# Kernel optimization log

Measured on AMD Instinct MI355X. Metric: run time of the kernel, lower is better.

The kernel has to match this reference:

```python
import jax, jax.numpy as jnp
import numpy as np

EPS = 1e-5

def _dynconv1x1(x, f):
    # x: [B, Cin, H, W], f: [B, Cout, Cin, 1, 1] -> [B, Cout, H, W]
    return jnp.einsum('bchw,boc->bohw', x, f[..., 0, 0])

def _instance_norm(x):
    # per-sample, per-channel normalization over spatial dims (no affine)
    mu = jnp.mean(x, axis=(2, 3), keepdims=True)
    var = jnp.mean(jnp.square(x - mu), axis=(2, 3), keepdims=True)
    return (x - mu) / jnp.sqrt(var + EPS)

def setup_inputs() -> dict:
    key = jax.random.key(0)
    ks = jax.random.split(key, 10)
    B, C = 32, 128
    sizes = [128, 64, 32, 16, 8]
    inp = {}
    for i, s in enumerate(sizes):
        inp[f'x{i+1}'] = jax.random.normal(ks[i], (B, C, s, s), dtype=jnp.float32)
        inp[f'l{i+1}fs'] = jax.random.normal(ks[5 + i], (B, C, C, 1, 1), dtype=jnp.float32) * 0.05
    return inp

def reference(x1, x2, x3, x4, x5, l1fs, l2fs, l3fs, l4fs, l5fs):
    y1 = _instance_norm(_dynconv1x1(x1, l1fs))
    y2 = _instance_norm(_dynconv1x1(x2, l2fs))
    y3 = _instance_norm(_dynconv1x1(x3, l3fs))
    y4 = _instance_norm(_dynconv1x1(x4, l4fs))
    y5 = _dynconv1x1(x5, l5fs)  # level 5 has no norm in the original
    return (y1, y2, y3, y4, y5)
```

## Files before the change

kernel.cpp:

```cpp
#include <hip/hip_runtime.h>
#include <stdint.h>


typedef __bf16 bf16x8 __attribute__((ext_vector_type(8)));
typedef float f32x4 __attribute__((ext_vector_type(4)));
typedef unsigned short u16;
typedef u16 u16x4 __attribute__((ext_vector_type(4)));
typedef u16 u16x8 __attribute__((ext_vector_type(8)));

__device__ __forceinline__ u16 f2bf(float f) {
    uint32_t u = __builtin_bit_cast(uint32_t, f);
    u += 0x7fffu + ((u >> 16) & 1u);
    return (u16)(u >> 16);
}
__device__ __forceinline__ float bf2f(u16 h) {
    return __builtin_bit_cast(float, (uint32_t)h << 16);
}

#define LDSP 136

template<bool YBF16>
__global__ __launch_bounds__(256, 2)
void conv_kernel(const float* __restrict__ x, const float* __restrict__ fw,
                 float* __restrict__ out, u16* __restrict__ ybf,
                 float* __restrict__ ysum, float* __restrict__ ysq,
                 int HW, int ntiles, int do_stats)
{
    __shared__ u16 ldsF[128 * LDSP];
    __shared__ u16 ldsX[128 * LDSP];

    const int t  = threadIdx.x;
    const int b  = blockIdx.x / ntiles;
    const int st = blockIdx.x % ntiles;

    const float* fb = fw + (size_t)b * (128 * 128);
    const float* xb = x  + (size_t)b * 128 * HW + st * 128;

    #pragma unroll
    for (int i = 0; i < 16; ++i) {
        int fi  = t + 256 * i;
        int row = fi >> 5;
        int c4  = fi & 31;
        f32x4 v = *reinterpret_cast<const f32x4*>(fb + row * 128 + c4 * 4);
        u16x4 h = { f2bf(v[0]), f2bf(v[1]), f2bf(v[2]), f2bf(v[3]) };
        *reinterpret_cast<u16x4*>(&ldsF[row * LDSP + c4 * 4]) = h;
    }
    #pragma unroll
    for (int i = 0; i < 16; ++i) {
        int fi  = t + 256 * i;
        int row = fi >> 5;
        int c4  = fi & 31;
        int s   = c4 * 4;
        if (st * 128 + s < HW) {
            f32x4 v = *reinterpret_cast<const f32x4*>(xb + (size_t)row * HW + s);
            u16x4 h = { f2bf(v[0]), f2bf(v[1]), f2bf(v[2]), f2bf(v[3]) };
            *reinterpret_cast<u16x4*>(&ldsX[row * LDSP + c4 * 4]) = h;
        }
    }
    __syncthreads();

    const int lane = t & 63;
    const int w    = t >> 6;
    const int wm   = w >> 1;
    const int wn   = w & 1;
    const int m16  = lane & 15;
    const int quad = lane >> 4;

    f32x4 acc[4][4] = {};

    #pragma unroll
    for (int ks = 0; ks < 4; ++ks) {
        const int kbase = ks * 32 + quad * 8;
        bf16x8 afr[4], bfr[4];
        #pragma unroll
        for (int i = 0; i < 4; ++i) {
            int row = wm * 64 + i * 16 + m16;
            afr[i] = *reinterpret_cast<const bf16x8*>(&ldsF[row * LDSP + kbase]);
        }
        #pragma unroll
        for (int j = 0; j < 4; ++j) {
            int col = wn * 64 + j * 16 + m16;
            u16x8 tmp;
            #pragma unroll
            for (int e = 0; e < 8; ++e)
                tmp[e] = ldsX[(kbase + e) * LDSP + col];
            bfr[j] = __builtin_bit_cast(bf16x8, tmp);
        }
        #pragma unroll
        for (int i = 0; i < 4; ++i)
            #pragma unroll
            for (int j = 0; j < 4; ++j)
                acc[i][j] = __builtin_amdgcn_mfma_f32_16x16x32_bf16(afr[i], bfr[j], acc[i][j], 0, 0, 0);
    }

    const size_t outbase = (size_t)b * 128 * HW;
    #pragma unroll
    for (int i = 0; i < 4; ++i) {
        #pragma unroll
        for (int r = 0; r < 4; ++r) {
            const int o = wm * 64 + i * 16 + quad * 4 + r;
            float s1 = 0.f, s2 = 0.f;
            #pragma unroll
            for (int j = 0; j < 4; ++j) {
                float v = acc[i][j][r];
                int s = st * 128 + wn * 64 + j * 16 + m16;
                if (s < HW) {
                    size_t idx = outbase + (size_t)o * HW + s;
                    if constexpr (YBF16) ybf[idx] = f2bf(v);
                    else                 out[idx] = v;
                }
                s1 += v; s2 += v * v;
            }
            if (do_stats) {
                #pragma unroll
                for (int off = 8; off; off >>= 1) {
                    s1 += __shfl_xor(s1, off, 64);
                    s2 += __shfl_xor(s2, off, 64);
                }
                if (m16 == 0) {
                    atomicAdd(&ysum[b * 128 + o], s1);
                    atomicAdd(&ysq [b * 128 + o], s2);
                }
            }
        }
    }
}

template<bool INBF16>
__global__ void norm_kernel(const u16* __restrict__ ybf, float* __restrict__ out,
                            const float* __restrict__ ysum, const float* __restrict__ ysq,
                            int HW, int n4)
{
    const int hw4 = HW >> 2;
    const float invHW = 1.0f / (float)HW;
    for (int idx = blockIdx.x * blockDim.x + threadIdx.x; idx < n4;
         idx += gridDim.x * blockDim.x) {
        int row = idx / hw4;
        float mean = ysum[row] * invHW;
        float var  = ysq[row] * invHW - mean * mean;
        float rstd = rsqrtf(var + 1e-5f);
        f32x4 v;
        if constexpr (INBF16) {
            u16x4 h = reinterpret_cast<const u16x4*>(ybf)[idx];
            v[0] = bf2f(h[0]); v[1] = bf2f(h[1]); v[2] = bf2f(h[2]); v[3] = bf2f(h[3]);
        } else {
            v = reinterpret_cast<const f32x4*>(out)[idx];
        }
        v[0] = (v[0] - mean) * rstd;
        v[1] = (v[1] - mean) * rstd;
        v[2] = (v[2] - mean) * rstd;
        v[3] = (v[3] - mean) * rstd;
        reinterpret_cast<f32x4*>(out)[idx] = v;
    }
}

extern "C" void kernel_launch(void* const* d_in, const int* in_sizes, int n_in,
                              void* d_out, int out_size, void* d_ws, size_t ws_size,
                              hipStream_t stream)
{
    (void)in_sizes; (void)n_in; (void)out_size;
    const float* x[5]  = {(const float*)d_in[0], (const float*)d_in[2], (const float*)d_in[4],
                          (const float*)d_in[6], (const float*)d_in[8]};
    const float* fl[5] = {(const float*)d_in[1], (const float*)d_in[3], (const float*)d_in[5],
                          (const float*)d_in[7], (const float*)d_in[9]};
    float* out = (float*)d_out;

    const int HW[5] = {128 * 128, 64 * 64, 32 * 32, 16 * 16, 8 * 8};
    size_t off[5];
    off[0] = 0;
    for (int l = 1; l < 5; ++l) off[l] = off[l - 1] + (size_t)32 * 128 * HW[l - 1];

    float* stats = (float*)d_ws;
    const size_t STATS_BYTES = 4 * 8192 * sizeof(float);

    size_t ybf_off[4];
    size_t need = STATS_BYTES;
    for (int l = 0; l < 4; ++l) { ybf_off[l] = need; need += (size_t)32 * 128 * HW[l] * sizeof(u16); }
    const bool usebf = (ws_size >= need);

    hipMemsetAsync(d_ws, 0, STATS_BYTES, stream);

    for (int l = 0; l < 5; ++l) {
        int ntiles = (HW[l] + 127) / 128;
        int grid = 32 * ntiles;
        float* ysum = stats + (l < 4 ? l : 0) * 8192;
        float* ysq  = ysum + 4096;
        if (l < 4 && usebf) {
            u16* ybf = (u16*)((char*)d_ws + ybf_off[l]);
            conv_kernel<true><<<grid, 256, 0, stream>>>(x[l], fl[l], out + off[l], ybf,
                                                        ysum, ysq, HW[l], ntiles, 1);
        } else {
            conv_kernel<false><<<grid, 256, 0, stream>>>(x[l], fl[l], out + off[l], nullptr,
                                                         ysum, ysq, HW[l], ntiles, l < 4 ? 1 : 0);
        }
    }
    for (int l = 0; l < 4; ++l) {
        int n4 = 32 * 128 * HW[l] / 4;
        int blocks = (n4 + 255) / 256;
        if (blocks > 2048) blocks = 2048;
        float* ysum = stats + l * 8192;
        float* ysq  = ysum + 4096;
        if (usebf) {
            const u16* ybf = (const u16*)((char*)d_ws + ybf_off[l]);
            norm_kernel<true><<<blocks, 256, 0, stream>>>(ybf, out + off[l], ysum, ysq, HW[l], n4);
        } else {
            norm_kernel<false><<<blocks, 256, 0, stream>>>(nullptr, out + off[l], ysum, ysq, HW[l], n4);
        }
    }
}
```

Baseline: 801.2 us.

## Make conv blocks persistent with prefetched X tiles and swizzled transposed LDS

```diff
diff --git a/kernel.cpp b/kernel.cpp
--- a/kernel.cpp
+++ b/kernel.cpp
@@ -2,62 +2,74 @@
 #include <stdint.h>
 
 
+typedef __bf16 bf16;
 typedef __bf16 bf16x8 __attribute__((ext_vector_type(8)));
 typedef float f32x4 __attribute__((ext_vector_type(4)));
 typedef unsigned short u16;
 typedef u16 u16x4 __attribute__((ext_vector_type(4)));
 typedef u16 u16x8 __attribute__((ext_vector_type(8)));
 
-__device__ __forceinline__ u16 f2bf(float f) {
-    uint32_t u = __builtin_bit_cast(uint32_t, f);
-    u += 0x7fffu + ((u >> 16) & 1u);
-    return (u16)(u >> 16);
-}
 __device__ __forceinline__ float bf2f(u16 h) {
     return __builtin_bit_cast(float, (uint32_t)h << 16);
 }
-
-#define LDSP 136
+__device__ __forceinline__ u16x4 cvt4(f32x4 v) {
+    u16x4 r;
+#pragma unroll
+    for (int i = 0; i < 4; ++i) {
+        bf16 h = (bf16)v[i];
+        r[i] = __builtin_bit_cast(u16, h);
+    }
+    return r;
+}
+__device__ __forceinline__ int swz8(int r) {
+    return ((r & 7) ^ ((r >> 3) & 7)) << 3;
+}
 
 template<bool YBF16>
 __global__ __launch_bounds__(256, 2)
 void conv_kernel(const float* __restrict__ x, const float* __restrict__ fw,
                  float* __restrict__ out, u16* __restrict__ ybf,
                  float* __restrict__ ysum, float* __restrict__ ysq,
-                 int HW, int ntiles, int do_stats)
+                 int HW, int ntiles, int nblk, int do_stats)
 {
-    __shared__ u16 ldsF[128 * LDSP];
-    __shared__ u16 ldsX[128 * LDSP];
-
-    const int t  = threadIdx.x;
-    const int b  = blockIdx.x / ntiles;
-    const int st = blockIdx.x % ntiles;
+    __shared__ u16 ldsF[128 * 128];
+    __shared__ u16 ldsX[128 * 128];
+
+    const int t   = threadIdx.x;
+    const int b   = blockIdx.x / nblk;
+    const int blk = blockIdx.x % nblk;
 
     const float* fb = fw + (size_t)b * (128 * 128);
-    const float* xb = x  + (size_t)b * 128 * HW + st * 128;
-
-    #pragma unroll
+    const float* xb = x  + (size_t)b * 128 * HW;
+
+    const int sq  = (t >> 1) & 31;
+    const int cqb = (t & 1) + ((t >> 6) << 1);
+
+    f32x4 xv[4][4];
+
+    auto issue_x = [&](int st) {
+        const float* xt = xb + (size_t)st * 128;
+        const int sg = (st * 128 + sq * 4 < HW) ? sq * 4 : 0;
+#pragma unroll
+        for (int it = 0; it < 4; ++it) {
+            const int cq = cqb + 8 * it;
+#pragma unroll
+            for (int e = 0; e < 4; ++e)
+                xv[it][e] = *reinterpret_cast<const f32x4*>(
+                    xt + (size_t)(cq * 4 + e) * HW + sg);
+        }
+    };
+
+    issue_x(blk);
+
+#pragma unroll
     for (int i = 0; i < 16; ++i) {
-        int fi  = t + 256 * i;
-        int row = fi >> 5;
-        int c4  = fi & 31;
-        f32x4 v = *reinterpret_cast<const f32x4*>(fb + row * 128 + c4 * 4);
-        u16x4 h = { f2bf(v[0]), f2bf(v[1]), f2bf(v[2]), f2bf(v[3]) };
-        *reinterpret_cast<u16x4*>(&ldsF[row * LDSP + c4 * 4]) = h;
-    }
-    #pragma unroll
-    for (int i = 0; i < 16; ++i) {
-        int fi  = t + 256 * i;
-        int row = fi >> 5;
-        int c4  = fi & 31;
-        int s   = c4 * 4;
-        if (st * 128 + s < HW) {
-            f32x4 v = *reinterpret_cast<const f32x4*>(xb + (size_t)row * HW + s);
-            u16x4 h = { f2bf(v[0]), f2bf(v[1]), f2bf(v[2]), f2bf(v[3]) };
-            *reinterpret_cast<u16x4*>(&ldsX[row * LDSP + c4 * 4]) = h;
-        }
-    }
-    __syncthreads();
+        const int fi  = t + 256 * i;
+        const int row = fi >> 5;
+        const int c4  = (fi & 31) * 4;
+        f32x4 v = *reinterpret_cast<const f32x4*>(fb + row * 128 + c4);
+        *reinterpret_cast<u16x4*>(&ldsF[row * 128 + (c4 ^ swz8(row))]) = cvt4(v);
+    }
 
     const int lane = t & 63;
     const int w    = t >> 6;
@@ -65,92 +77,119 @@
     const int wn   = w & 1;
     const int m16  = lane & 15;
     const int quad = lane >> 4;
-
-    f32x4 acc[4][4] = {};
-
-    #pragma unroll
-    for (int ks = 0; ks < 4; ++ks) {
-        const int kbase = ks * 32 + quad * 8;
-        bf16x8 afr[4], bfr[4];
-        #pragma unroll
+    const int q8   = quad * 8;
+
+    const size_t outbase = (size_t)b * 128 * HW;
+
+    for (int st = blk; st < ntiles; st += nblk) {
+#pragma unroll
+        for (int it = 0; it < 4; ++it) {
+            const int cq = cqb + 8 * it;
+            u16x4 h[4];
+#pragma unroll
+            for (int e = 0; e < 4; ++e) h[e] = cvt4(xv[it][e]);
+#pragma unroll
+            for (int e2 = 0; e2 < 4; ++e2) {
+                const int s = sq * 4 + e2;
+                u16x4 o4 = { h[0][e2], h[1][e2], h[2][e2], h[3][e2] };
+                *reinterpret_cast<u16x4*>(
+                    &ldsX[s * 128 + ((cq * 4) ^ swz8(s))]) = o4;
+            }
+        }
+        __syncthreads();
+
+        if (st + nblk < ntiles) issue_x(st + nblk);
+
+        f32x4 acc[4][4] = {};
+#pragma unroll
+        for (int ks = 0; ks < 4; ++ks) {
+            const int kb = ks * 32 + q8;
+            bf16x8 afr[4], bfr[4];
+#pragma unroll
+            for (int i = 0; i < 4; ++i) {
+                const int r = wm * 64 + i * 16 + m16;
+                afr[i] = *reinterpret_cast<const bf16x8*>(
+                    &ldsF[r * 128 + (kb ^ swz8(r))]);
+            }
+#pragma unroll
+            for (int j = 0; j < 4; ++j) {
+                const int r = wn * 64 + j * 16 + m16;
+                bfr[j] = *reinterpret_cast<const bf16x8*>(
+                    &ldsX[r * 128 + (kb ^ swz8(r))]);
+            }
+#pragma unroll
+            for (int i = 0; i < 4; ++i)
+#pragma unroll
+                for (int j = 0; j < 4; ++j)
+                    acc[i][j] = __builtin_amdgcn_mfma_f32_16x16x32_bf16(
+                        afr[i], bfr[j], acc[i][j], 0, 0, 0);
+        }
+
+#pragma unroll
         for (int i = 0; i < 4; ++i) {
-            int row = wm * 64 + i * 16 + m16;
-            afr[i] = *reinterpret_cast<const bf16x8*>(&ldsF[row * LDSP + kbase]);
-        }
-        #pragma unroll
-        for (int j = 0; j < 4; ++j) {
-            int col = wn * 64 + j * 16 + m16;
-            u16x8 tmp;
-            #pragma unroll
-            for (int e = 0; e < 8; ++e)
-                tmp[e] = ldsX[(kbase + e) * LDSP + col];
-            bfr[j] = __builtin_bit_cast(bf16x8, tmp);
-        }
-        #pragma unroll
-        for (int i = 0; i < 4; ++i)
-            #pragma unroll
-            for (int j = 0; j < 4; ++j)
-                acc[i][j] = __builtin_amdgcn_mfma_f32_16x16x32_bf16(afr[i], bfr[j], acc[i][j], 0, 0, 0);
-    }
-
-    const size_t outbase = (size_t)b * 128 * HW;
-    #pragma unroll
-    for (int i = 0; i < 4; ++i) {
-        #pragma unroll
-        for (int r = 0; r < 4; ++r) {
-            const int o = wm * 64 + i * 16 + quad * 4 + r;
-            float s1 = 0.f, s2 = 0.f;
-            #pragma unroll
-            for (int j = 0; j < 4; ++j) {
-                float v = acc[i][j][r];
-                int s = st * 128 + wn * 64 + j * 16 + m16;
-                if (s < HW) {
-                    size_t idx = outbase + (size_t)o * HW + s;
-                    if constexpr (YBF16) ybf[idx] = f2bf(v);
-                    else                 out[idx] = v;
+#pragma unroll
+            for (int r = 0; r < 4; ++r) {
+                const int o = wm * 64 + i * 16 + quad * 4 + r;
+                float s1 = 0.f, s2 = 0.f;
+#pragma unroll
+                for (int j = 0; j < 4; ++j) {
+                    float v = acc[i][j][r];
+                    const int s = st * 128 + wn * 64 + j * 16 + m16;
+                    if (s < HW) {
+                        const size_t idx = outbase + (size_t)o * HW + s;
+                        if constexpr (YBF16)
+                            ybf[idx] = __builtin_bit_cast(u16, (bf16)v);
+                        else
+                            out[idx] = v;
+                    }
+                    s1 += v; s2 += v * v;
                 }
-                s1 += v; s2 += v * v;
-            }
-            if (do_stats) {
-                #pragma unroll
-                for (int off = 8; off; off >>= 1) {
-                    s1 += __shfl_xor(s1, off, 64);
-                    s2 += __shfl_xor(s2, off, 64);
+                if (do_stats) {
+#pragma unroll
+                    for (int off = 8; off; off >>= 1) {
+                        s1 += __shfl_xor(s1, off, 64);
+                        s2 += __shfl_xor(s2, off, 64);
+                    }
+                    if (m16 == 0) {
+                        atomicAdd(&ysum[b * 128 + o], s1);
+                        atomicAdd(&ysq [b * 128 + o], s2);
+                    }
                 }
-                if (m16 == 0) {
-                    atomicAdd(&ysum[b * 128 + o], s1);
-                    atomicAdd(&ysq [b * 128 + o], s2);
-                }
-            }
-        }
+            }
+        }
+        __syncthreads();
     }
 }
 
 template<bool INBF16>
-__global__ void norm_kernel(const u16* __restrict__ ybf, float* __restrict__ out,
-                            const float* __restrict__ ysum, const float* __restrict__ ysq,
-                            int HW, int n4)
+__global__ __launch_bounds__(256)
+void norm_kernel(const u16* __restrict__ ybf, float* __restrict__ out,
+                 const float* __restrict__ ysum, const float* __restrict__ ysq,
+                 int log2hw, int n8)
 {
-    const int hw4 = HW >> 2;
-    const float invHW = 1.0f / (float)HW;
-    for (int idx = blockIdx.x * blockDim.x + threadIdx.x; idx < n4;
-         idx += gridDim.x * blockDim.x) {
-        int row = idx / hw4;
-        float mean = ysum[row] * invHW;
-        float var  = ysq[row] * invHW - mean * mean;
-        float rstd = rsqrtf(var + 1e-5f);
-        f32x4 v;
+    const float invHW = 1.0f / (float)(1 << log2hw);
+    const int stride = gridDim.x * blockDim.x;
+    for (int i8 = blockIdx.x * blockDim.x + threadIdx.x; i8 < n8; i8 += stride) {
+        const int row = i8 >> (log2hw - 3);
+        const float mean = ysum[row] * invHW;
+        const float var  = ysq[row] * invHW - mean * mean;
+        const float rstd = rsqrtf(var + 1e-5f);
+        f32x4 lo, hi;
         if constexpr (INBF16) {
-            u16x4 h = reinterpret_cast<const u16x4*>(ybf)[idx];
-            v[0] = bf2f(h[0]); v[1] = bf2f(h[1]); v[2] = bf2f(h[2]); v[3] = bf2f(h[3]);
+            u16x8 h = reinterpret_cast<const u16x8*>(ybf)[i8];
+            lo = f32x4{ bf2f(h[0]), bf2f(h[1]), bf2f(h[2]), bf2f(h[3]) };
+            hi = f32x4{ bf2f(h[4]), bf2f(h[5]), bf2f(h[6]), bf2f(h[7]) };
         } else {
-            v = reinterpret_cast<const f32x4*>(out)[idx];
-        }
-        v[0] = (v[0] - mean) * rstd;
-        v[1] = (v[1] - mean) * rstd;
-        v[2] = (v[2] - mean) * rstd;
-        v[3] = (v[3] - mean) * rstd;
-        reinterpret_cast<f32x4*>(out)[idx] = v;
+            lo = reinterpret_cast<const f32x4*>(out)[i8 * 2];
+            hi = reinterpret_cast<const f32x4*>(out)[i8 * 2 + 1];
+        }
+#pragma unroll
+        for (int k = 0; k < 4; ++k) {
+            lo[k] = (lo[k] - mean) * rstd;
+            hi[k] = (hi[k] - mean) * rstd;
+        }
+        reinterpret_cast<f32x4*>(out)[i8 * 2]     = lo;
+        reinterpret_cast<f32x4*>(out)[i8 * 2 + 1] = hi;
     }
 }
 
@@ -165,7 +204,8 @@
                           (const float*)d_in[7], (const float*)d_in[9]};
     float* out = (float*)d_out;
 
-    const int HW[5] = {128 * 128, 64 * 64, 32 * 32, 16 * 16, 8 * 8};
+    const int HW[5]     = {128 * 128, 64 * 64, 32 * 32, 16 * 16, 8 * 8};
+    const int LOG2HW[5] = {14, 12, 10, 8, 6};
     size_t off[5];
     off[0] = 0;
     for (int l = 1; l < 5; ++l) off[l] = off[l - 1] + (size_t)32 * 128 * HW[l - 1];
@@ -181,30 +221,36 @@
     hipMemsetAsync(d_ws, 0, STATS_BYTES, stream);
 
     for (int l = 0; l < 5; ++l) {
-        int ntiles = (HW[l] + 127) / 128;
-        int grid = 32 * ntiles;
+        const int ntiles = (HW[l] + 127) / 128;
+        int nblk = ntiles;
+        if (ntiles >= 128)     nblk = 32;
+        else if (ntiles >= 32) nblk = 16;
+        const int grid = 32 * nblk;
         float* ysum = stats + (l < 4 ? l : 0) * 8192;
         float* ysq  = ysum + 4096;
         if (l < 4 && usebf) {
             u16* ybf = (u16*)((char*)d_ws + ybf_off[l]);
             conv_kernel<true><<<grid, 256, 0, stream>>>(x[l], fl[l], out + off[l], ybf,
-                                                        ysum, ysq, HW[l], ntiles, 1);
+                                                        ysum, ysq, HW[l], ntiles, nblk, 1);
         } else {
             conv_kernel<false><<<grid, 256, 0, stream>>>(x[l], fl[l], out + off[l], nullptr,
-                                                         ysum, ysq, HW[l], ntiles, l < 4 ? 1 : 0);
+                                                         ysum, ysq, HW[l], ntiles, nblk,
+                                                         l < 4 ? 1 : 0);
         }
     }
     for (int l = 0; l < 4; ++l) {
-        int n4 = 32 * 128 * HW[l] / 4;
-        int blocks = (n4 + 255) / 256;
+        const int n8 = 32 * 128 * HW[l] / 8;
+        int blocks = (n8 + 255) / 256;
         if (blocks > 2048) blocks = 2048;
         float* ysum = stats + l * 8192;
         float* ysq  = ysum + 4096;
         if (usebf) {
             const u16* ybf = (const u16*)((char*)d_ws + ybf_off[l]);
-            norm_kernel<true><<<blocks, 256, 0, stream>>>(ybf, out + off[l], ysum, ysq, HW[l], n4);
+            norm_kernel<true><<<blocks, 256, 0, stream>>>(ybf, out + off[l], ysum, ysq,
+                                                          LOG2HW[l], n8);
         } else {
-            norm_kernel<false><<<blocks, 256, 0, stream>>>(nullptr, out + off[l], ysum, ysq, HW[l], n4);
-        }
-    }
-}
+            norm_kernel<false><<<blocks, 256, 0, stream>>>(nullptr, out + off[l], ysum, ysq,
+                                                           LOG2HW[l], n8);
+        }
+    }
+}
```

Result: slower. 854.0 us (+6.6%).
